# Performance work log

Hardware: AMD Instinct MI355X
Metric: run time of the kernel (lower is better)

The kernel has to match this reference:

```python
import jax, jax.numpy as jnp
import numpy as np


def setup_inputs() -> dict:
    key = jax.random.key(0)
    k0, k1, k2, k3 = jax.random.split(key, 4)
    B, L, D, H = 8, 4096, 300, 128  # batch, leaves (power of 2), embed dim, hidden
    x = jax.random.normal(k0, (B, L, D), jnp.float32)
    W_leaf = jax.random.normal(k1, (D, 2 * H), jnp.float32) * (1.0 / np.sqrt(D))
    b_leaf = jnp.zeros((2 * H,), jnp.float32)
    W_l = jax.random.normal(k2, (H, 5 * H), jnp.float32) * (1.0 / np.sqrt(H))
    W_r = jax.random.normal(k3, (H, 5 * H), jnp.float32) * (1.0 / np.sqrt(H))
    b = jnp.zeros((5 * H,), jnp.float32)
    return {"x": x, "W_leaf": W_leaf, "b_leaf": b_leaf, "W_l": W_l, "W_r": W_r, "b": b}


def reference(x, W_leaf, b_leaf, W_l, W_r, b):
    """Binary TreeLSTM over a complete tree: leaves -> root.

    x: [B, L, D] leaf embeddings, L a power of 2.
    Leaf transform: linear projection split into (h, c) (SPINN-style).
    REDUCE: 5-gate child-sum-of-two composition.
    Returns root hidden state: [B, H].
    """
    H = W_l.shape[0]
    hc = x @ W_leaf + b_leaf                     # [B, L, 2H]
    h, c = hc[..., :H], hc[..., H:]
    levels = int(np.log2(x.shape[1]))
    for _ in range(levels):                      # level-batched tree reduction
        h_l, h_r = h[:, 0::2], h[:, 1::2]        # [B, n/2, H]
        c_l, c_r = c[:, 0::2], c[:, 1::2]
        gates = h_l @ W_l + h_r @ W_r + b        # [B, n/2, 5H]
        i, fl, fr, o, g = jnp.split(gates, 5, axis=-1)
        c = (jax.nn.sigmoid(fl) * c_l
             + jax.nn.sigmoid(fr) * c_r
             + jax.nn.sigmoid(i) * jnp.tanh(g))
        h = jax.nn.sigmoid(o) * jnp.tanh(c)
    return h[:, 0]                               # root hidden state [B, H]
```

## Files before the change

### kernel.cpp

```cpp
#include <hip/hip_runtime.h>
#include <hip/hip_bf16.h>
#include <math.h>


typedef __attribute__((ext_vector_type(8))) short bfrag8;
typedef __attribute__((ext_vector_type(4))) float f32x4;

__device__ __forceinline__ float rcpf(float x) { return __builtin_amdgcn_rcpf(x); }
__device__ __forceinline__ float sigf(float x) { return rcpf(1.0f + __expf(-x)); }
__device__ __forceinline__ float tanh_f(float x) {
    float e = __expf(2.0f * x);
    return 1.0f - 2.0f * rcpf(e + 1.0f);
}
__device__ __forceinline__ short f2bf(float f) {
    __hip_bfloat16 h = __float2bfloat16(f);
    return *reinterpret_cast<short*>(&h);
}
__device__ __forceinline__ bfrag8 pack8(f32x4 a, f32x4 b) {
    union { int i[4]; bfrag8 v; } u;
    asm("v_cvt_pk_bf16_f32 %0, %1, %2" : "=v"(u.i[0]) : "v"(a[0]), "v"(a[1]));
    asm("v_cvt_pk_bf16_f32 %0, %1, %2" : "=v"(u.i[1]) : "v"(a[2]), "v"(a[3]));
    asm("v_cvt_pk_bf16_f32 %0, %1, %2" : "=v"(u.i[2]) : "v"(b[0]), "v"(b[1]));
    asm("v_cvt_pk_bf16_f32 %0, %1, %2" : "=v"(u.i[3]) : "v"(b[2]), "v"(b[3]));
    return u.v;
}
#define GLDS(gp, lp) __builtin_amdgcn_global_load_lds( \
    (const __attribute__((address_space(1))) void*)(gp), \
    (__attribute__((address_space(3))) void*)(lp), 16, 0, 0)

__global__ __launch_bounds__(256) void reorder_kernel(
    const float* __restrict__ W_l, const float* __restrict__ W_r,
    const float* __restrict__ W_leaf,
    short* __restrict__ Wcat_ch, short* __restrict__ Wleaf_ch)
{
    int idx = blockIdx.x * 256 + threadIdx.x;
    if (idx < 163840) {
        int n = idx >> 8, k = idx & 255;
        float v = (k < 128) ? W_l[k * 640 + n] : W_r[(k - 128) * 640 + n];
        Wcat_ch[(((size_t)(k >> 3)) * 640 + n) * 8 + (k & 7)] = f2bf(v);
        return;
    }
    idx -= 163840;
    if (idx < 81920) {
        int n = idx / 320, k = idx - n * 320;
        short v = (k < 300) ? f2bf(W_leaf[k * 256 + n]) : (short)0;
        Wleaf_ch[(((size_t)(k >> 3)) * 256 + n) * 8 + (k & 7)] = v;
    }
}

__global__ __launch_bounds__(256) void leaf_kernel(
    const float* __restrict__ x, const short* __restrict__ Bw,
    const float* __restrict__ bleaf,
    short* __restrict__ hD,
    float* __restrict__ cD)
{
    __shared__ float Als[128 * 64];
    __shared__ short Bls[8 * 128 * 8];
    const int tid  = threadIdx.x;
    const int w    = tid >> 6, lane = tid & 63;
    const int quad = lane >> 4, l16 = lane & 15;
    const int mBlk = blockIdx.x * 128, nBlk = blockIdx.y * 128;
    const int waveM = (w >> 1) * 64, waveN = (w & 1) * 64;

    f32x4 acc[4][4] = {};
    const f32x4 zero4 = {0.f, 0.f, 0.f, 0.f};

    for (int c = 0; c < 5; ++c) {
        const int k0 = c * 64;
        {
            const int q_lds = lane & 15;
            const int rsub  = lane >> 4;
            #pragma unroll
            for (int g = 0; g < 8; ++g) {
                int row = w * 32 + g * 4 + rsub;
                int q_g = (q_lds & 8) | ((q_lds & 7) ^ (row & 7));
                if (c < 4 || q_g < 11) {
                    GLDS(x + (size_t)(mBlk + row) * 300 + k0 + q_g * 4,
                         (char*)Als + (w * 32 + g * 4) * 256);
                } else {
                    *(f32x4*)((char*)Als + row * 256 + q_lds * 16) = zero4;
                }
            }
        }
        #pragma unroll
        for (int g2 = 0; g2 < 4; ++g2) {
            int u = w * 4 + g2;
            GLDS(Bw + ((size_t)(c * 8 + (u >> 1)) * 256 + nBlk + (u & 1) * 64 + lane) * 8,
                 (char*)Bls + u * 1024);
        }
        __syncthreads();
        #pragma unroll
        for (int ks = 0; ks < 2; ++ks) {
            const int ca = ks * 4 + quad;
            bfrag8 af[4], bf4[4];
            #pragma unroll
            for (int i = 0; i < 4; ++i) {
                int r  = waveM + i * 16 + l16;
                int u0 = 2 * ca, u1 = 2 * ca + 1;
                int s0 = (u0 & 8) | ((u0 & 7) ^ (r & 7));
                int s1 = (u1 & 8) | ((u1 & 7) ^ (r & 7));
                f32x4 a0 = *(const f32x4*)(Als + r * 64 + s0 * 4);
                f32x4 a1 = *(const f32x4*)(Als + r * 64 + s1 * 4);
                af[i] = pack8(a0, a1);
            }
            #pragma unroll
            for (int jn = 0; jn < 4; ++jn)
                bf4[jn] = *(const bfrag8*)(Bls + (ca * 128 + waveN + jn * 16 + l16) * 8);
            #pragma unroll
            for (int i = 0; i < 4; ++i)
                #pragma unroll
                for (int jn = 0; jn < 4; ++jn)
                    acc[i][jn] = __builtin_amdgcn_mfma_f32_16x16x32_bf16(
                                     af[i], bf4[jn], acc[i][jn], 0, 0, 0);
        }
        __syncthreads();
    }

    #pragma unroll
    for (int i = 0; i < 4; ++i) {
        int row0 = mBlk + waveM + i * 16 + quad * 4;
        #pragma unroll
        for (int jn = 0; jn < 4; ++jn) {
            int col = nBlk + waveN + jn * 16 + l16;
            float bv = bleaf[col];
            #pragma unroll
            for (int rg = 0; rg < 4; ++rg) {
                float v = acc[i][jn][rg] + bv;
                int m = row0 + rg;
                if (nBlk == 0) {
                    int hc = col;
                    hD[(((size_t)((m & 1) * 16 + (hc >> 3))) * 16384 + (m >> 1)) * 8
                       + (hc & 7)] = f2bf(v);
                } else {
                    cD[(size_t)m * 128 + (col - 128)] = v;
                }
            }
        }
    }
}

__global__ __launch_bounds__(256, 2) void level_ws_kernel(
    const short* __restrict__ A,
    const float* __restrict__ cprev,
    const short* __restrict__ Wch,
    const float* __restrict__ bias,
    short* __restrict__ hout, float* __restrict__ cout_,
    int M)
{
    __shared__ short Als[32 * 64 * 8];
    const int tid  = threadIdx.x;
    const int w    = tid >> 6, lane = tid & 63;
    const int quad = lane >> 4, l16 = lane & 15;
    const int j  = blockIdx.y;
    const int tb = blockIdx.x * 64;
    const int h  = j * 16 + l16;

    {
        int row = tb + lane; if (row >= M) row = 0;
        #pragma unroll
        for (int s = 0; s < 8; ++s)
            GLDS(A + ((size_t)(s * 4 + w) * M + row) * 8,
                 (char*)Als + (s * 4 + w) * 1024);
    }

    bfrag8 Wfr[5][8];
    #pragma unroll
    for (int g = 0; g < 5; ++g)
        #pragma unroll
        for (int s = 0; s < 8; ++s)
            Wfr[g][s] = *(const bfrag8*)(Wch + ((size_t)(s * 4 + quad) * 640
                                                + g * 128 + h) * 8);
    const float bi  = bias[h],       bfl = bias[128 + h], bfr_ = bias[256 + h];
    const float bo  = bias[384 + h], bg  = bias[512 + h];

    __syncthreads();

    f32x4 acc[5] = {};
    #pragma unroll
    for (int s = 0; s < 8; ++s) {
        bfrag8 af = *(const bfrag8*)(Als + ((s * 4 + quad) * 64 + w * 16 + l16) * 8);
        #pragma unroll
        for (int g = 0; g < 5; ++g)
            acc[g] = __builtin_amdgcn_mfma_f32_16x16x32_bf16(af, Wfr[g][s], acc[g], 0, 0, 0);
    }

    const int Mn = M >> 1;
    #pragma unroll
    for (int rg = 0; rg < 4; ++rg) {
        int m = tb + w * 16 + quad * 4 + rg;
        if (m < M) {
            float gi  = acc[0][rg] + bi;
            float gfl = acc[1][rg] + bfl;
            float gfr = acc[2][rg] + bfr_;
            float go  = acc[3][rg] + bo;
            float gg  = acc[4][rg] + bg;
            float cl  = cprev[(size_t)(2 * m) * 128 + h];
            float cr  = cprev[(size_t)(2 * m + 1) * 128 + h];
            float cn  = sigf(gfl) * cl + sigf(gfr) * cr + sigf(gi) * tanh_f(gg);
            float hn  = sigf(go) * tanh_f(cn);
            hout[(((size_t)((m & 1) * 16 + (h >> 3))) * Mn + (m >> 1)) * 8
                 + (h & 7)] = f2bf(hn);
            cout_[(size_t)m * 128 + h] = cn;
        }
    }
}

__global__ __launch_bounds__(512) void finish_kernel(
    const short* __restrict__ hin,
    const float* __restrict__ cin,
    const short* __restrict__ Wch, const float* __restrict__ bias,
    float* __restrict__ out)
{
    __shared__ short hP[32 * 64 * 8];
    __shared__ short hQ[32 * 32 * 8];
    __shared__ float cA[128 * 128];
    __shared__ float cB[64 * 128];
    const int tid  = threadIdx.x;
    const int w    = tid >> 6, lane = tid & 63;
    const int quad = lane >> 4, l16 = lane & 15;
    const int h    = w * 16 + l16;

    #pragma unroll
    for (int g = 0; g < 4; ++g)
        GLDS(hin + ((size_t)((g * 8 + w) * 64 + lane)) * 8,
             (char*)hP + ((g * 8 + w) * 64) * 16);
    #pragma unroll
    for (int g = 0; g < 8; ++g)
        GLDS(cin + ((size_t)((g * 8 + w) * 64 + lane)) * 4,
             (char*)cA + ((g * 8 + w) * 64) * 16);

    bfrag8 Wfr[5][8];
    #pragma unroll
    for (int g = 0; g < 5; ++g)
        #pragma unroll
        for (int s = 0; s < 8; ++s)
            Wfr[g][s] = *(const bfrag8*)(Wch + ((size_t)(s * 4 + quad) * 640
                                                + g * 128 + h) * 8);
    const float bi  = bias[h],       bfl = bias[128 + h], bfr_ = bias[256 + h];
    const float bo  = bias[384 + h], bg  = bias[512 + h];

    __syncthreads();

    #pragma unroll
    for (int t = 0; t < 4; ++t) {
        const int Mo = 64 >> t;
        const short* hsrc = (t & 1) ? hQ : hP;
        short* hdst       = (t & 1) ? hP : hQ;
        const float* cread = (t & 1) ? cB : cA;
        float*       cwrite = (t & 1) ? cA : cB;
        const int nrt = (Mo + 15) >> 4;

        for (int rt = 0; rt < nrt; ++rt) {
            f32x4 acc[5] = {};
            #pragma unroll
            for (int s = 0; s < 8; ++s) {
                bfrag8 af = *(const bfrag8*)(hsrc + ((s * 4 + quad) * Mo
                                                     + rt * 16 + l16) * 8);
                #pragma unroll
                for (int g = 0; g < 5; ++g)
                    acc[g] = __builtin_amdgcn_mfma_f32_16x16x32_bf16(
                                 af, Wfr[g][s], acc[g], 0, 0, 0);
            }
            #pragma unroll
            for (int rg = 0; rg < 4; ++rg) {
                int m = rt * 16 + quad * 4 + rg;
                if (m < Mo) {
                    float gi  = acc[0][rg] + bi;
                    float gfl = acc[1][rg] + bfl;
                    float gfr = acc[2][rg] + bfr_;
                    float go  = acc[3][rg] + bo;
                    float gg  = acc[4][rg] + bg;
                    float cl  = cread[(2 * m) * 128 + h];
                    float cr  = cread[(2 * m + 1) * 128 + h];
                    float cn  = sigf(gfl) * cl + sigf(gfr) * cr + sigf(gi) * tanh_f(gg);
                    float hn  = sigf(go) * tanh_f(cn);
                    if (t == 3) {
                        out[(size_t)m * 128 + h] = hn;
                    } else {
                        hdst[(((m & 1) * 16 + (h >> 3)) * (Mo >> 1) + (m >> 1)) * 8
                             + (h & 7)] = f2bf(hn);
                        cwrite[m * 128 + h] = cn;
                    }
                }
            }
        }
        __syncthreads();
    }
}

extern "C" void kernel_launch(void* const* d_in, const int* in_sizes, int n_in,
                              void* d_out, int out_size, void* d_ws, size_t ws_size,
                              hipStream_t stream)
{
    const float* x      = (const float*)d_in[0];
    const float* W_leaf = (const float*)d_in[1];
    const float* b_leaf = (const float*)d_in[2];
    const float* W_l    = (const float*)d_in[3];
    const float* W_r    = (const float*)d_in[4];
    const float* b      = (const float*)d_in[5];
    float* out = (float*)d_out;

    char* p = (char*)d_ws;
    short* hA    = (short*)p; p += (size_t)32 * 16384 * 16 + 1024;
    short* hB    = (short*)p; p += (size_t)32 * 8192 * 16 + 1024;
    float* c0    = (float*)p; p += (size_t)32768 * 128 * 4;
    float* c1    = (float*)p; p += (size_t)16384 * 128 * 4;
    short* WcatC = (short*)p; p += (size_t)32 * 640 * 16;
    short* WlfC  = (short*)p; p += (size_t)40 * 256 * 16;

    reorder_kernel<<<960, 256, 0, stream>>>(W_l, W_r, W_leaf, WcatC, WlfC);
    leaf_kernel<<<dim3(256, 2), 256, 0, stream>>>(x, WlfC, b_leaf, hA, c0);

    const short* hin = hA; const float* cin = c0;
    int M = 16384;
    for (int lev = 1; lev <= 8; ++lev) {
        short* ho = (lev & 1) ? hB : hA;
        float* co = (lev & 1) ? c1 : c0;
        level_ws_kernel<<<dim3((M + 63) / 64, 8), 256, 0, stream>>>(
            hin, cin, WcatC, b, ho, co, M);
        hin = ho; cin = co;
        M >>= 1;
    }
    finish_kernel<<<1, 512, 0, stream>>>(hA, c0, WcatC, b, out);
}
```

Before: 186.8 us.

## Fuse pairs of tree levels into one kernel with LDS-resident intermediates

```diff
diff --git a/kernel.cpp b/kernel.cpp
--- a/kernel.cpp
+++ b/kernel.cpp
@@ -139,29 +139,24 @@
     }
 }
 
-__global__ __launch_bounds__(256, 2) void level_ws_kernel(
+__global__ __launch_bounds__(512, 2) void fused2_kernel(
     const short* __restrict__ A,
     const float* __restrict__ cprev,
     const short* __restrict__ Wch,
     const float* __restrict__ bias,
-    short* __restrict__ hout, float* __restrict__ cout_,
-    int M)
+    short* __restrict__ hout,
+    float* __restrict__ cout_,
+    int M2)
 {
     __shared__ short Als[32 * 64 * 8];
+    __shared__ short hL [128 * 128];
+    __shared__ float cL [128 * 128];
     const int tid  = threadIdx.x;
     const int w    = tid >> 6, lane = tid & 63;
     const int quad = lane >> 4, l16 = lane & 15;
-    const int j  = blockIdx.y;
-    const int tb = blockIdx.x * 64;
-    const int h  = j * 16 + l16;
-
-    {
-        int row = tb + lane; if (row >= M) row = 0;
-        #pragma unroll
-        for (int s = 0; s < 8; ++s)
-            GLDS(A + ((size_t)(s * 4 + w) * M + row) * 8,
-                 (char*)Als + (s * 4 + w) * 1024);
-    }
+    const int h    = w * 16 + l16;
+    const int M1   = M2 * 2;
+    const int Lbase = blockIdx.x * 128;
 
     bfrag8 Wfr[5][8];
     #pragma unroll
@@ -173,34 +168,76 @@
     const float bi  = bias[h],       bfl = bias[128 + h], bfr_ = bias[256 + h];
     const float bo  = bias[384 + h], bg  = bias[512 + h];
 
-    __syncthreads();
-
-    f32x4 acc[5] = {};
-    #pragma unroll
-    for (int s = 0; s < 8; ++s) {
-        bfrag8 af = *(const bfrag8*)(Als + ((s * 4 + quad) * 64 + w * 16 + l16) * 8);
-        #pragma unroll
-        for (int g = 0; g < 5; ++g)
-            acc[g] = __builtin_amdgcn_mfma_f32_16x16x32_bf16(af, Wfr[g][s], acc[g], 0, 0, 0);
-    }
-
-    const int Mn = M >> 1;
-    #pragma unroll
-    for (int rg = 0; rg < 4; ++rg) {
-        int m = tb + w * 16 + quad * 4 + rg;
-        if (m < M) {
+    for (int st = 0; st < 2; ++st) {
+        #pragma unroll
+        for (int s = 0; s < 4; ++s)
+            GLDS(A + ((size_t)(s * 8 + w) * M1 + Lbase + st * 64 + lane) * 8,
+                 (char*)Als + (s * 8 + w) * 1024);
+        __syncthreads();
+
+        for (int rt = 0; rt < 4; ++rt) {
+            f32x4 acc[5] = {};
+            #pragma unroll
+            for (int s = 0; s < 8; ++s) {
+                bfrag8 af = *(const bfrag8*)(Als + ((s * 4 + quad) * 64
+                                                    + rt * 16 + l16) * 8);
+                #pragma unroll
+                for (int g = 0; g < 5; ++g)
+                    acc[g] = __builtin_amdgcn_mfma_f32_16x16x32_bf16(
+                                 af, Wfr[g][s], acc[g], 0, 0, 0);
+            }
+            #pragma unroll
+            for (int rg = 0; rg < 4; ++rg) {
+                int mloc = rt * 16 + quad * 4 + rg;
+                int mG   = Lbase + st * 64 + mloc;
+                float gi  = acc[0][rg] + bi;
+                float gfl = acc[1][rg] + bfl;
+                float gfr = acc[2][rg] + bfr_;
+                float go  = acc[3][rg] + bo;
+                float gg  = acc[4][rg] + bg;
+                float cl  = cprev[(size_t)(2 * mG) * 128 + h];
+                float cr  = cprev[(size_t)(2 * mG + 1) * 128 + h];
+                float cn  = sigf(gfl) * cl + sigf(gfr) * cr + sigf(gi) * tanh_f(gg);
+                float hn  = sigf(go) * tanh_f(cn);
+                int row = st * 64 + mloc;
+                cL[row * 128 + h] = cn;
+                int byte = (row * 256 + h * 2) ^ (((row >> 1) & 7) << 4);
+                *(short*)((char*)hL + byte) = f2bf(hn);
+            }
+        }
+        __syncthreads();
+    }
+
+    const int Mn2 = M2 >> 1;
+    for (int rt = 0; rt < 4; ++rt) {
+        f32x4 acc[5] = {};
+        #pragma unroll
+        for (int s = 0; s < 8; ++s) {
+            int c    = s * 4 + quad;
+            int row  = 2 * (rt * 16 + l16) + (c >> 4);
+            int byte = (row * 256 + (c & 15) * 16) ^ (((row >> 1) & 7) << 4);
+            bfrag8 af = *(const bfrag8*)((const char*)hL + byte);
+            #pragma unroll
+            for (int g = 0; g < 5; ++g)
+                acc[g] = __builtin_amdgcn_mfma_f32_16x16x32_bf16(
+                             af, Wfr[g][s], acc[g], 0, 0, 0);
+        }
+        #pragma unroll
+        for (int rg = 0; rg < 4; ++rg) {
+            int mloc = rt * 16 + quad * 4 + rg;
+            int m2   = blockIdx.x * 64 + mloc;
             float gi  = acc[0][rg] + bi;
             float gfl = acc[1][rg] + bfl;
             float gfr = acc[2][rg] + bfr_;
             float go  = acc[3][rg] + bo;
             float gg  = acc[4][rg] + bg;
-            float cl  = cprev[(size_t)(2 * m) * 128 + h];
-            float cr  = cprev[(size_t)(2 * m + 1) * 128 + h];
+            float cl  = cL[(2 * mloc) * 128 + h];
+            float cr  = cL[(2 * mloc + 1) * 128 + h];
             float cn  = sigf(gfl) * cl + sigf(gfr) * cr + sigf(gi) * tanh_f(gg);
             float hn  = sigf(go) * tanh_f(cn);
-            hout[(((size_t)((m & 1) * 16 + (h >> 3))) * Mn + (m >> 1)) * 8
+            hout[(((size_t)((m2 & 1) * 16 + (h >> 3))) * Mn2 + (m2 >> 1)) * 8
                  + (h & 7)] = f2bf(hn);
-            cout_[(size_t)m * 128 + h] = cn;
+            cout_[(size_t)m2 * 128 + h] = cn;
         }
     }
 }
@@ -246,7 +283,7 @@
         const int Mo = 64 >> t;
         const short* hsrc = (t & 1) ? hQ : hP;
         short* hdst       = (t & 1) ? hP : hQ;
-        const float* cread = (t & 1) ? cB : cA;
+        const float* cread  = (t & 1) ? cB : cA;
         float*       cwrite = (t & 1) ? cA : cB;
         const int nrt = (Mo + 15) >> 4;
 
@@ -311,15 +348,10 @@
     reorder_kernel<<<960, 256, 0, stream>>>(W_l, W_r, W_leaf, WcatC, WlfC);
     leaf_kernel<<<dim3(256, 2), 256, 0, stream>>>(x, WlfC, b_leaf, hA, c0);
 
-    const short* hin = hA; const float* cin = c0;
-    int M = 16384;
-    for (int lev = 1; lev <= 8; ++lev) {
-        short* ho = (lev & 1) ? hB : hA;
-        float* co = (lev & 1) ? c1 : c0;
-        level_ws_kernel<<<dim3((M + 63) / 64, 8), 256, 0, stream>>>(
-            hin, cin, WcatC, b, ho, co, M);
-        hin = ho; cin = co;
-        M >>= 1;
-    }
+    fused2_kernel<<<128, 512, 0, stream>>>(hA, c0, WcatC, b, hB, c1, 8192);
+    fused2_kernel<<< 32, 512, 0, stream>>>(hB, c1, WcatC, b, hA, c0, 2048);
+    fused2_kernel<<<  8, 512, 0, stream>>>(hA, c0, WcatC, b, hB, c1,  512);
+    fused2_kernel<<<  2, 512, 0, stream>>>(hB, c1, WcatC, b, hA, c0,  128);
+
     finish_kernel<<<1, 512, 0, stream>>>(hA, c0, WcatC, b, out);
 }
```

Measured after the change: 226.7 us. +21.4%, slower.
